# Optimization experiments

Measured on AMD Instinct MI355X. Metric: run time of the kernel, lower is better.

## Reference

```python
import jax, jax.numpy as jnp
import numpy as np

B, N, OBS, H, A = 1024, 64, 128, 256, 16
NH = 4
HD = H // NH


def _linear_params(key, fan_in, fan_out):
    k1, k2 = jax.random.split(key)
    bound = 1.0 / np.sqrt(fan_in)
    W = jax.random.uniform(k1, (fan_out, fan_in), jnp.float32, -bound, bound)
    b = jax.random.uniform(k2, (fan_out,), jnp.float32, -bound, bound)
    return W, b


def setup_inputs() -> dict:
    key = jax.random.key(0)
    ks = jax.random.split(key, 10)
    obs = jax.random.normal(ks[0], (B, N, OBS), jnp.float32)
    adj = jax.random.randint(ks[1], (B, N, N), 0, 2).astype(jnp.float32)
    # guarantee every row has at least one neighbor (self-loop) so softmax is finite
    adj = jnp.maximum(adj, jnp.eye(N, dtype=jnp.float32)[None])
    W1, b1 = _linear_params(ks[2], OBS, H)
    W2, b2 = _linear_params(ks[3], H, H)
    Wq, bq = _linear_params(ks[4], H, H)
    Wk, bk = _linear_params(ks[5], H, H)
    Wv, bv = _linear_params(ks[6], H, H)
    Wo, bo = _linear_params(ks[7], H, H)
    Wc, bc = _linear_params(ks[8], H, H)
    W3, b3 = _linear_params(ks[9], H, A)
    return dict(obs=obs, adj=adj, W1=W1, b1=b1, W2=W2, b2=b2,
                Wq=Wq, bq=bq, Wk=Wk, bk=bk, Wv=Wv, bv=bv,
                Wo=Wo, bo=bo, Wc=Wc, bc=bc, W3=W3, b3=b3)


def reference(obs, adj, W1, b1, W2, b2, Wq, bq, Wk, bk, Wv, bv, Wo, bo, Wc, bc, W3, b3):
    lin = lambda x, W, b: jnp.einsum('bnd,od->bno', x, W) + b
    x = jax.nn.relu(lin(obs, W1, b1))
    x = jax.nn.relu(lin(x, W2, b2))
    # multi-head attention with adjacency mask
    def heads(t):  # [B,N,H] -> [B,NH,N,HD]
        return t.reshape(B, N, NH, HD).transpose(0, 2, 1, 3)
    q = heads(lin(x, Wq, bq))
    k = heads(lin(x, Wk, bk))
    v = heads(lin(x, Wv, bv))
    scores = jnp.einsum('bhqd,bhkd->bhqk', q, k) / np.sqrt(HD).astype(np.float32)
    scores = jnp.where(adj[:, None] == 0, -jnp.inf, scores)
    attn = jax.nn.softmax(scores, axis=-1)
    out = jnp.einsum('bhqk,bhkd->bhqd', attn, v)
    out = out.transpose(0, 2, 1, 3).reshape(B, N, H)
    x = lin(out, Wo, bo)
    # communication: adj @ fc(x)
    x = jnp.einsum('bnm,bmh->bnh', adj, lin(x, Wc, bc))
    return lin(x, W3, b3)
```

## Files before the change

kernel.cpp:

```cpp
#include <hip/hip_runtime.h>
#include <stdint.h>

typedef unsigned short u16;
typedef unsigned long long u64;
typedef __attribute__((ext_vector_type(8))) short short8;
typedef __attribute__((ext_vector_type(4))) float f32x4;

#define MFMA16 __builtin_amdgcn_mfma_f32_16x16x32_bf16

#define MTOT 65536

__device__ __forceinline__ u16 f2bf(float f) {
  union { float f; uint32_t u; } v; v.f = f;
  uint32_t r = v.u + 0x7FFFu + ((v.u >> 16) & 1u);
  return (u16)(r >> 16);
}

union U8 { short8 v; u16 u[8]; };
union U4 { u64 v; u16 u[4]; };

__device__ __forceinline__ void cp16(const void* g, void* l) {
  __builtin_amdgcn_global_load_lds(
      (const __attribute__((address_space(1))) void*)g,
      (__attribute__((address_space(3))) void*)l, 16, 0, 0);
}

__device__ __forceinline__ int swz(int row) { return ((row >> 1) & 3) << 4; }

__global__ __launch_bounds__(256) void k_l1(
    const float* __restrict__ Wc, const float* __restrict__ Wo,
    const float* __restrict__ bo, const float* __restrict__ bc,
    float* __restrict__ M1, float* __restrict__ bv,
    const float* __restrict__ W1, const float* __restrict__ W2,
    const float* __restrict__ Wq, const float* __restrict__ Wk,
    u16* o1, u16* o2, u16* oq, u16* ok,
    const float* __restrict__ adj, u64* __restrict__ adjm_g) {
  const int bid = blockIdx.x, tid = threadIdx.x;
  if (bid < 256) {
    __shared__ float wcr[256];
    __shared__ float red[4];
    const int j = bid, d = tid;
    wcr[d] = Wc[j * 256 + d];
    __syncthreads();
    float acc = 0.f;
#pragma unroll 8
    for (int i = 0; i < 256; i++) acc += wcr[i] * Wo[i * 256 + d];
    M1[j * 256 + d] = acc;
    float p = wcr[d] * bo[d];
    for (int off = 32; off >= 1; off >>= 1) p += __shfl_xor(p, off);
    if ((d & 63) == 0) red[d >> 6] = p;
    __syncthreads();
    if (d == 0) bv[j] = bc[j] + red[0] + red[1] + red[2] + red[3];
  } else if (bid < 368) {
    int off8 = (bid - 256) * 256 + tid;
    const float* src; u16* dst;
    if      (off8 <  4096) { src = W1; dst = o1; }
    else if (off8 < 12288) { src = W2; dst = o2; off8 -= 4096; }
    else if (off8 < 20480) { src = Wq; dst = oq; off8 -= 12288; }
    else                   { src = Wk; dst = ok; off8 -= 20480; }
    const int e = off8 * 8;
    f32x4 a = *(const f32x4*)(src + e);
    f32x4 b = *(const f32x4*)(src + e + 4);
    U8 pk;
#pragma unroll
    for (int j = 0; j < 4; j++) { pk.u[j] = f2bf(a[j]); pk.u[4 + j] = f2bf(b[j]); }
    *(short8*)(dst + e) = pk.v;
  } else {
    __shared__ u16 chunk[64][4];
    const int b = bid - 368;
    const int q = tid >> 2, qa = tid & 3;
    const float* ar = adj + ((size_t)b * 64 + q) * 64 + qa * 16;
    f32x4 a0 = *(const f32x4*)(ar);
    f32x4 a1 = *(const f32x4*)(ar + 4);
    f32x4 a2 = *(const f32x4*)(ar + 8);
    f32x4 a3 = *(const f32x4*)(ar + 12);
    unsigned m16 = 0;
#pragma unroll
    for (int i = 0; i < 4; i++) {
      m16 |= (unsigned)(a0[i] != 0.f) << i;
      m16 |= (unsigned)(a1[i] != 0.f) << (4 + i);
      m16 |= (unsigned)(a2[i] != 0.f) << (8 + i);
      m16 |= (unsigned)(a3[i] != 0.f) << (12 + i);
    }
    chunk[q][qa] = (u16)m16;
    __syncthreads();
    if (tid < 64)
      adjm_g[(size_t)b * 64 + tid] =
          (u64)chunk[tid][0] | ((u64)chunk[tid][1] << 16) |
          ((u64)chunk[tid][2] << 32) | ((u64)chunk[tid][3] << 48);
  }
}

template<int K, bool AF32, bool VZ>
__device__ __forceinline__ void gemm_full2(
    const void* __restrict__ Ain, const u16* __restrict__ W,
    const float* __restrict__ bias, u16* __restrict__ C,
    const int m0, const bool relu, char* smem,
    const u16* __restrict__ Gw, u16* __restrict__ Vzt) {
  const int tid = threadIdx.x;
  const int lane = tid & 63, wid = tid >> 6;
  const int wr = wid >> 1, wc = wid & 1;
  const int ro = lane & 15, hi = lane >> 4;

  f32x4 acc0[4][4], acc1[4][4];
#pragma unroll
  for (int m = 0; m < 4; m++)
#pragma unroll
    for (int n = 0; n < 4; n++) {
      acc0[m][n] = (f32x4){0.f, 0.f, 0.f, 0.f};
      acc1[m][n] = (f32x4){0.f, 0.f, 0.f, 0.f};
    }
  f32x4 vzacc[2][4];
  if (VZ) {
#pragma unroll
    for (int h = 0; h < 2; h++)
#pragma unroll
      for (int cf = 0; cf < 4; cf++) vzacc[h][cf] = (f32x4){0.f, 0.f, 0.f, 0.f};
  }

  auto stage = [&](int buf, int k0) {
    char* Ax = smem + buf * 24576;
    char* Bx = Ax + 8192;
    if (AF32) {
      const float* Af = (const float*)Ain;
#pragma unroll
      for (int it = 0; it < 2; it++) {
        const int e = (tid + it * 256) * 8;
        const int r = e >> 5, c = e & 31;
        const float* s = Af + (size_t)(m0 + r) * K + k0 + c;
        f32x4 a = *(const f32x4*)s, b = *(const f32x4*)(s + 4);
        U8 pk;
#pragma unroll
        for (int j = 0; j < 4; j++) { pk.u[j] = f2bf(a[j]); pk.u[4 + j] = f2bf(b[j]); }
        *(short8*)(Ax + ((r * 64 + c * 2) ^ swz(r))) = pk.v;
      }
    } else {
      const u16* Ab = (const u16*)Ain;
#pragma unroll
      for (int i = 0; i < 2; i++) {
        const int boff = i * 4096 + wid * 1024;
        const int t = boff + lane * 16;
        const int row = t >> 6;
        const int cb = (t & 63) ^ swz(row);
        cp16(Ab + (size_t)(m0 + row) * K + k0 + (cb >> 1), Ax + boff);
      }
    }
#pragma unroll
    for (int i = 0; i < 4; i++) {
      const int boff = i * 4096 + wid * 1024;
      const int t = boff + lane * 16;
      const int row = t >> 6;
      const int cb = (t & 63) ^ swz(row);
      cp16(W + (size_t)row * K + k0 + (cb >> 1), Bx + boff);
    }
  };

  auto compute = [&](int buf) {
    char* Ax = smem + buf * 24576;
    char* Bx = Ax + 8192;
    short8 af[4], fb0[4], fb1[4];
#pragma unroll
    for (int m = 0; m < 4; m++) {
      const int row = wr * 64 + m * 16 + ro;
      af[m] = *(const short8*)(Ax + ((row * 64 + hi * 16) ^ swz(row)));
    }
#pragma unroll
    for (int n = 0; n < 4; n++) {
      const int r0 = wc * 64 + n * 16 + ro;
      fb0[n] = *(const short8*)(Bx + ((r0 * 64 + hi * 16) ^ swz(r0)));
      const int r1 = 128 + r0;
      fb1[n] = *(const short8*)(Bx + ((r1 * 64 + hi * 16) ^ swz(r1)));
    }
    __builtin_amdgcn_s_setprio(1);
#pragma unroll
    for (int m = 0; m < 4; m++)
#pragma unroll
      for (int n = 0; n < 4; n++) {
        acc0[m][n] = MFMA16(af[m], fb0[n], acc0[m][n], 0, 0, 0);
        acc1[m][n] = MFMA16(af[m], fb1[n], acc1[m][n], 0, 0, 0);
      }
    __builtin_amdgcn_s_setprio(0);
  };

  constexpr int NT = K / 32;
  if (AF32) {
    stage(0, 0);
    __syncthreads();
    int cur = 0;
    for (int k0 = 32; k0 < K; k0 += 32) {
      stage(cur ^ 1, k0);
      compute(cur);
      __syncthreads();
      cur ^= 1;
    }
    compute(cur);
    __syncthreads();
  } else {
    stage(0, 0);
    stage(1, 32);
#pragma unroll
    for (int t = 0; t < NT; ++t) {
      if (t == NT - 1) asm volatile("s_waitcnt vmcnt(0)" ::: "memory");
      else             asm volatile("s_waitcnt vmcnt(6)" ::: "memory");
      asm volatile("s_barrier" ::: "memory");
      compute(t & 1);
      asm volatile("s_barrier" ::: "memory");
      if (t + 2 < NT) stage(t & 1, (t + 2) * 32);
    }
  }

  u16 (*Cs)[136] = (u16(*)[136])smem;
  char* Gl = smem + 18432;
  auto ep = [&](f32x4 (&acc)[4][4], const int n0) {
    if (VZ) {
#pragma unroll
      for (int i = 0; i < 4; i++) {
        const int boff = i * 4096 + wid * 1024;
        const int t = boff + lane * 16;
        const int row = t >> 8;
        const int cb = (t & 255) ^ ((row & 7) << 4);
        cp16(Gw + (size_t)row * 256 + n0 + (cb >> 1), Gl + boff);
      }
    }
#pragma unroll
    for (int half = 0; half < 2; half++) {
      if (wr == half) {
#pragma unroll
        for (int n = 0; n < 4; n++) {
          const int col = wc * 64 + n * 16 + ro;
          const float bb = bias[n0 + col];
#pragma unroll
          for (int m = 0; m < 4; m++)
#pragma unroll
            for (int j = 0; j < 4; j++) {
              float val = acc[m][n][j] + bb;
              if (relu) val = fmaxf(val, 0.f);
              Cs[m * 16 + hi * 4 + j][col] = f2bf(val);
            }
        }
      }
      __syncthreads();
      for (int i = tid; i < 64 * 16; i += 256) {
        const int r = i >> 4, c = (i & 15) << 3;
        *(short8*)(C + (size_t)(m0 + half * 64 + r) * 256 + n0 + c) = *(short8*)&Cs[r][c];
      }
      if (VZ) {
#pragma unroll
        for (int ks = 0; ks < 4; ks++) {
          short8 af = *(const short8*)&Cs[wid * 16 + ro][ks * 32 + hi * 8];
#pragma unroll
          for (int cf = 0; cf < 4; cf++) {
            const int c = cf * 16 + ro;
            short8 gb = *(const short8*)(Gl + ((c * 256 + (ks * 32 + hi * 8) * 2) ^ ((c & 7) << 4)));
            vzacc[half][cf] = MFMA16(af, gb, vzacc[half][cf], 0, 0, 0);
          }
        }
      }
      __syncthreads();
    }
  };
  ep(acc0, 0);
  ep(acc1, 128);

  if (VZ) {
#pragma unroll
    for (int half = 0; half < 2; half++) {
      const int bidx = (m0 >> 6) + half;
      const int ke = wid * 16 + hi * 4;
#pragma unroll
      for (int cf = 0; cf < 4; cf++) {
        const int c = cf * 16 + ro;
        U4 pk;
#pragma unroll
        for (int j = 0; j < 4; j++) pk.u[j] = f2bf(vzacc[half][cf][j]);
        *(u64*)(Vzt + (size_t)bidx * 4096 + (size_t)c * 64 + ke) = pk.v;
      }
    }
  }
}

__global__ __launch_bounds__(256, 2) void k_gemm1_prep2(
    const float* __restrict__ obs, const u16* __restrict__ W1b,
    const float* __restrict__ b1, u16* __restrict__ x1,
    const float* __restrict__ W3, const float* __restrict__ M1,
    const float* __restrict__ bvchain, const float* __restrict__ bvw,
    const float* __restrict__ Wv, u16* __restrict__ G,
    float* __restrict__ bz) {
  __shared__ char smem[49152];
  if (blockIdx.x < 512) {
    gemm_full2<128, true, false>(obs, W1b, b1, x1, (int)blockIdx.x * 128,
                                 true, smem, nullptr, nullptr);
    return;
  }
  float* w3r = (float*)smem;
  float* wzs = (float*)(smem + 1024);
  float* red = (float*)(smem + 2048);
  const int a = blockIdx.x - 512, d = threadIdx.x;
  w3r[d] = W3[a * 256 + d];
  __syncthreads();
  float acc = 0.f;
#pragma unroll 8
  for (int j = 0; j < 256; j++) acc += w3r[j] * M1[j * 256 + d];
  wzs[d] = acc;
  float p = w3r[d] * bvchain[d] + acc * bvw[d];
  for (int off = 32; off >= 1; off >>= 1) p += __shfl_xor(p, off);
  if ((d & 63) == 0) red[d >> 6] = p;
  __syncthreads();
  if (d == 0) bz[a] = red[0] + red[1] + red[2] + red[3];
#pragma unroll
  for (int h = 0; h < 4; h++) {
    float g = 0.f;
#pragma unroll 8
    for (int d2 = 0; d2 < 64; d2++)
      g += wzs[h * 64 + d2] * Wv[(size_t)(h * 64 + d2) * 256 + d];
    G[(size_t)(h * 16 + a) * 256 + d] = f2bf(g);
  }
}

__global__ __launch_bounds__(256, 2) void k_x2_vz(
    const u16* __restrict__ x1, const u16* __restrict__ W2b,
    const float* __restrict__ b2, u16* __restrict__ x2,
    const u16* __restrict__ G, u16* __restrict__ Vzt) {
  __shared__ char smem[49152];
  gemm_full2<256, false, true>(x1, W2b, b2, x2, (int)blockIdx.x * 128,
                               true, smem, G, Vzt);
}

__global__ __launch_bounds__(256, 2) void k_qk(
    const u16* __restrict__ x2,
    const u16* __restrict__ Wqb, const float* __restrict__ bq, u16* __restrict__ Qg,
    const u16* __restrict__ Wkb, const float* __restrict__ bk, u16* __restrict__ Kg) {
  __shared__ char smem[49152];
  const int bid = blockIdx.x;
  const int q = bid >> 4, r = bid & 15;
  const int mt = q * 8 + (r & 7);
  const int sub = r >> 3;
  gemm_full2<256, false, false>(x2, sub ? Wkb : Wqb, sub ? bk : bq,
                                sub ? Kg : Qg, mt * 128, false, smem,
                                nullptr, nullptr);
}

__global__ __launch_bounds__(256, 2) void attn_fused(
    const u16* __restrict__ Qg, const u16* __restrict__ Kg,
    const u16* __restrict__ Vzt, const u64* __restrict__ adjm_g,
    const float* __restrict__ bz, const float* __restrict__ b3,
    float* __restrict__ out) {
  __shared__ char sm_raw[36864];
  __shared__ u64 adjm[64];
  u16 (*Ps)[64][72] = (u16(*)[64][72])sm_raw;
  float (*Zs)[64][16] = (float(*)[64][16])sm_raw;

  const int b = blockIdx.x, tid = threadIdx.x;
  const int lane = tid & 63, w = tid >> 6;
  const int ro = lane & 15, hi = lane >> 4;
  const int hc = w * 64;
  const size_t base = (size_t)b * 64 * 256;

  if (tid < 64) adjm[tid] = adjm_g[(size_t)b * 64 + tid];

  short8 kb[4][2];
#pragma unroll
  for (int n = 0; n < 4; n++)
#pragma unroll
    for (int ks = 0; ks < 2; ks++)
      kb[n][ks] = *(const short8*)(Kg + base + (size_t)(n * 16 + ro) * 256 + hc + ks * 32 + hi * 8);

  f32x4 s[4][4];
#pragma unroll
  for (int m = 0; m < 4; m++) {
    short8 af[2];
#pragma unroll
    for (int ks = 0; ks < 2; ks++)
      af[ks] = *(const short8*)(Qg + base + (size_t)(m * 16 + ro) * 256 + hc + ks * 32 + hi * 8);
#pragma unroll
    for (int n = 0; n < 4; n++) s[m][n] = (f32x4){0.f, 0.f, 0.f, 0.f};
#pragma unroll
    for (int ks = 0; ks < 2; ks++)
#pragma unroll
      for (int n = 0; n < 4; n++)
        s[m][n] = MFMA16(af[ks], kb[n][ks], s[m][n], 0, 0, 0);
  }

  short8 vz[2];
#pragma unroll
  for (int ks = 0; ks < 2; ks++)
    vz[ks] = *(const short8*)(Vzt + (size_t)b * 4096 + (size_t)(hc / 4 + ro) * 64 + ks * 32 + hi * 8);

  __syncthreads();

#pragma unroll
  for (int m = 0; m < 4; m++) {
#pragma unroll
    for (int j = 0; j < 4; j++) {
      const int q = m * 16 + hi * 4 + j;
      const u64 msk = adjm[q];
      float sv[4], ev[4];
      float mx = -3.0e38f;
#pragma unroll
      for (int n = 0; n < 4; n++) {
        const bool on = (msk >> (n * 16 + ro)) & 1ull;
        sv[n] = on ? s[m][n][j] * 0.125f : -3.0e38f;
        mx = fmaxf(mx, sv[n]);
      }
      mx = fmaxf(mx, __shfl_xor(mx, 1));
      mx = fmaxf(mx, __shfl_xor(mx, 2));
      mx = fmaxf(mx, __shfl_xor(mx, 4));
      mx = fmaxf(mx, __shfl_xor(mx, 8));
      float sum = 0.f;
#pragma unroll
      for (int n = 0; n < 4; n++) {
        ev[n] = (sv[n] > -1.0e37f) ? __expf(sv[n] - mx) : 0.f;
        sum += ev[n];
      }
      sum += __shfl_xor(sum, 1);
      sum += __shfl_xor(sum, 2);
      sum += __shfl_xor(sum, 4);
      sum += __shfl_xor(sum, 8);
      const float inv = 1.0f / sum;
#pragma unroll
      for (int n = 0; n < 4; n++)
        Ps[w][q][n * 16 + ro] = f2bf(ev[n] * inv);
    }
  }

  f32x4 oz[4];
#pragma unroll
  for (int m = 0; m < 4; m++) {
    short8 pa[2];
    pa[0] = *(const short8*)&Ps[w][m * 16 + ro][hi * 8];
    pa[1] = *(const short8*)&Ps[w][m * 16 + ro][32 + hi * 8];
    oz[m] = (f32x4){0.f, 0.f, 0.f, 0.f};
#pragma unroll
    for (int ks = 0; ks < 2; ks++)
      oz[m] = MFMA16(pa[ks], vz[ks], oz[m], 0, 0, 0);
  }
  __syncthreads();

#pragma unroll
  for (int m = 0; m < 4; m++)
#pragma unroll
    for (int j = 0; j < 4; j++)
      Zs[w][m * 16 + hi * 4 + j][ro] = oz[m][j];
  __syncthreads();

  for (int i = tid; i < 1024; i += 256) {
    const int r = i >> 4, a = i & 15;
    Zs[0][r][a] += Zs[1][r][a] + Zs[2][r][a] + Zs[3][r][a];
  }
  __syncthreads();

  {
    const int n = tid >> 2, a4 = (tid & 3) << 2;
    const u64 msk = adjm[n];
    const float deg = (float)__popcll(msk);
    float a0 = 0.f, a1 = 0.f, a2 = 0.f, a3 = 0.f;
#pragma unroll 8
    for (int m = 0; m < 64; m++) {
      const float wv = (float)((msk >> m) & 1ull);
      f32x4 z = *(const f32x4*)&Zs[0][m][a4];
      a0 += wv * z[0]; a1 += wv * z[1]; a2 += wv * z[2]; a3 += wv * z[3];
    }
    f32x4 r;
    r[0] = a0 + b3[a4 + 0] + deg * bz[a4 + 0];
    r[1] = a1 + b3[a4 + 1] + deg * bz[a4 + 1];
    r[2] = a2 + b3[a4 + 2] + deg * bz[a4 + 2];
    r[3] = a3 + b3[a4 + 3] + deg * bz[a4 + 3];
    *(f32x4*)(out + ((size_t)b * 64 + n) * 16 + a4) = r;
  }
}

extern "C" void kernel_launch(void* const* d_in, const int* in_sizes, int n_in,
                              void* d_out, int out_size, void* d_ws, size_t ws_size,
                              hipStream_t stream) {
  const float* obs = (const float*)d_in[0];
  const float* adj = (const float*)d_in[1];
  const float* W1  = (const float*)d_in[2];
  const float* b1  = (const float*)d_in[3];
  const float* W2  = (const float*)d_in[4];
  const float* b2  = (const float*)d_in[5];
  const float* Wq  = (const float*)d_in[6];
  const float* bq  = (const float*)d_in[7];
  const float* Wk  = (const float*)d_in[8];
  const float* bk  = (const float*)d_in[9];
  const float* Wv  = (const float*)d_in[10];
  const float* bvw = (const float*)d_in[11];
  const float* Wo  = (const float*)d_in[12];
  const float* bo  = (const float*)d_in[13];
  const float* Wc  = (const float*)d_in[14];
  const float* bc  = (const float*)d_in[15];
  const float* W3  = (const float*)d_in[16];
  const float* b3  = (const float*)d_in[17];
  float* out = (float*)d_out;

  char* ws = (char*)d_ws;
  const size_t BIG = (size_t)MTOT * 256 * 2;
  u16* buf0 = (u16*)(ws);
  u16* buf1 = (u16*)(ws + BIG);
  u16* buf2 = (u16*)(ws + 2 * BIG);
  u16* buf3 = (u16*)(ws + 3 * BIG);
  char* p = ws + 4 * BIG;
  u16* W1b = (u16*)p;              p += 128 * 256 * 2;
  u16* W2b = (u16*)p;              p += 256 * 256 * 2;
  u16* Wqb = (u16*)p;              p += 256 * 256 * 2;
  u16* Wkb = (u16*)p;              p += 256 * 256 * 2;
  float* M1 = (float*)p;           p += 256 * 256 * 4;
  u16* G   = (u16*)p;              p += 64 * 256 * 2;
  float* bv = (float*)p;           p += 256 * 4;
  float* bz = (float*)p;           p += 16 * 4;
  u64* adjm_g = (u64*)p;           p += (size_t)MTOT * 8;
  u16* Vzt = (u16*)p;              p += (size_t)MTOT * 64 * 2;

  dim3 blk(256);
  k_l1<<<dim3(1392), blk, 0, stream>>>(Wc, Wo, bo, bc, M1, bv,
                                       W1, W2, Wq, Wk, W1b, W2b, Wqb, Wkb,
                                       adj, adjm_g);
  k_gemm1_prep2<<<dim3(528), blk, 0, stream>>>(obs, W1b, b1, buf0,
                                               W3, M1, bv, bvw, Wv, G, bz);
  k_x2_vz<<<dim3(512), blk, 0, stream>>>(buf0, W2b, b2, buf1, G, Vzt);
  k_qk<<<dim3(1024), blk, 0, stream>>>(buf1, Wqb, bq, buf2, Wkb, bk, buf3);
  attn_fused<<<dim3(1024), blk, 0, stream>>>(buf2, buf3, Vzt, adjm_g, bz, b3, out);
}
```

Baseline: 130.1 us.

## Move Vz projection into Q-GEMM main loop and split G precompute across kernels

The Vz = x2·Gᵀ product was computed in the x2 GEMM epilogue from freshly written bf16 tiles. It now runs inside the K-loop of the Q-projection blocks in k_qk, reusing the already loaded x2 A-fragments with G tiles staged alongside the weights. The G matrix computation is split: Wz is stored to global in the prep kernel and G is built by extra blocks in the x2 kernel. This shortens the x2 epilogue and spreads the small prep work, but Q blocks do extra MFMAs and loads, and shared memory rises to 56KB, which may limit occupancy.

```diff
diff --git a/kernel.cpp b/kernel.cpp
--- a/kernel.cpp
+++ b/kernel.cpp
@@ -110,12 +110,12 @@
       acc0[m][n] = (f32x4){0.f, 0.f, 0.f, 0.f};
       acc1[m][n] = (f32x4){0.f, 0.f, 0.f, 0.f};
     }
-  f32x4 vzacc[2][4];
+  f32x4 vzacc[4][2];
   if (VZ) {
 #pragma unroll
-    for (int h = 0; h < 2; h++)
-#pragma unroll
-      for (int cf = 0; cf < 4; cf++) vzacc[h][cf] = (f32x4){0.f, 0.f, 0.f, 0.f};
+    for (int m = 0; m < 4; m++)
+#pragma unroll
+      for (int cf = 0; cf < 2; cf++) vzacc[m][cf] = (f32x4){0.f, 0.f, 0.f, 0.f};
   }
 
   auto stage = [&](int buf, int k0) {
@@ -153,6 +153,14 @@
       const int cb = (t & 63) ^ swz(row);
       cp16(W + (size_t)row * K + k0 + (cb >> 1), Bx + boff);
     }
+    if (VZ) {
+      char* Gx = smem + 49152 + buf * 4096;
+      const int boff = wid * 1024;
+      const int t = boff + lane * 16;
+      const int row = t >> 6;
+      const int cb = (t & 63) ^ swz(row);
+      cp16(Gw + (size_t)row * 256 + k0 + (cb >> 1), Gx + boff);
+    }
   };
 
   auto compute = [&](int buf) {
@@ -179,6 +187,17 @@
         acc0[m][n] = MFMA16(af[m], fb0[n], acc0[m][n], 0, 0, 0);
         acc1[m][n] = MFMA16(af[m], fb1[n], acc1[m][n], 0, 0, 0);
       }
+    if (VZ) {
+      char* Gx = smem + 49152 + buf * 4096;
+#pragma unroll
+      for (int cf = 0; cf < 2; cf++) {
+        const int row = wc * 32 + cf * 16 + ro;
+        short8 gb = *(const short8*)(Gx + ((row * 64 + hi * 16) ^ swz(row)));
+#pragma unroll
+        for (int m = 0; m < 4; m++)
+          vzacc[m][cf] = MFMA16(af[m], gb, vzacc[m][cf], 0, 0, 0);
+      }
+    }
     __builtin_amdgcn_s_setprio(0);
   };
 
@@ -200,8 +219,9 @@
     stage(1, 32);
 #pragma unroll
     for (int t = 0; t < NT; ++t) {
-      if (t == NT - 1) asm volatile("s_waitcnt vmcnt(0)" ::: "memory");
-      else             asm volatile("s_waitcnt vmcnt(6)" ::: "memory");
+      if (t == NT - 1)  asm volatile("s_waitcnt vmcnt(0)" ::: "memory");
+      else if (VZ)      asm volatile("s_waitcnt vmcnt(7)" ::: "memory");
+      else              asm volatile("s_waitcnt vmcnt(6)" ::: "memory");
       asm volatile("s_barrier" ::: "memory");
       compute(t & 1);
       asm volatile("s_barrier" ::: "memory");
@@ -209,19 +229,24 @@
     }
   }
 
+  if (VZ) {
+#pragma unroll
+    for (int m = 0; m < 4; m++) {
+      const int bidx = (m0 >> 6) + wr;
+      const int ke = m * 16 + hi * 4;
+#pragma unroll
+      for (int cf = 0; cf < 2; cf++) {
+        const int c = wc * 32 + cf * 16 + ro;
+        U4 pk;
+#pragma unroll
+        for (int j = 0; j < 4; j++) pk.u[j] = f2bf(vzacc[m][cf][j]);
+        *(u64*)(Vzt + (size_t)bidx * 4096 + (size_t)c * 64 + ke) = pk.v;
+      }
+    }
+  }
+
   u16 (*Cs)[136] = (u16(*)[136])smem;
-  char* Gl = smem + 18432;
   auto ep = [&](f32x4 (&acc)[4][4], const int n0) {
-    if (VZ) {
-#pragma unroll
-      for (int i = 0; i < 4; i++) {
-        const int boff = i * 4096 + wid * 1024;
-        const int t = boff + lane * 16;
-        const int row = t >> 8;
-        const int cb = (t & 255) ^ ((row & 7) << 4);
-        cp16(Gw + (size_t)row * 256 + n0 + (cb >> 1), Gl + boff);
-      }
-    }
 #pragma unroll
     for (int half = 0; half < 2; half++) {
       if (wr == half) {
@@ -244,39 +269,11 @@
         const int r = i >> 4, c = (i & 15) << 3;
         *(short8*)(C + (size_t)(m0 + half * 64 + r) * 256 + n0 + c) = *(short8*)&Cs[r][c];
       }
-      if (VZ) {
-#pragma unroll
-        for (int ks = 0; ks < 4; ks++) {
-          short8 af = *(const short8*)&Cs[wid * 16 + ro][ks * 32 + hi * 8];
-#pragma unroll
-          for (int cf = 0; cf < 4; cf++) {
-            const int c = cf * 16 + ro;
-            short8 gb = *(const short8*)(Gl + ((c * 256 + (ks * 32 + hi * 8) * 2) ^ ((c & 7) << 4)));
-            vzacc[half][cf] = MFMA16(af, gb, vzacc[half][cf], 0, 0, 0);
-          }
-        }
-      }
       __syncthreads();
     }
   };
   ep(acc0, 0);
   ep(acc1, 128);
-
-  if (VZ) {
-#pragma unroll
-    for (int half = 0; half < 2; half++) {
-      const int bidx = (m0 >> 6) + half;
-      const int ke = wid * 16 + hi * 4;
-#pragma unroll
-      for (int cf = 0; cf < 4; cf++) {
-        const int c = cf * 16 + ro;
-        U4 pk;
-#pragma unroll
-        for (int j = 0; j < 4; j++) pk.u[j] = f2bf(vzacc[half][cf][j]);
-        *(u64*)(Vzt + (size_t)bidx * 4096 + (size_t)c * 64 + ke) = pk.v;
-      }
-    }
-  }
 }
 
 __global__ __launch_bounds__(256, 2) void k_gemm1_prep2(
@@ -284,8 +281,7 @@
     const float* __restrict__ b1, u16* __restrict__ x1,
     const float* __restrict__ W3, const float* __restrict__ M1,
     const float* __restrict__ bvchain, const float* __restrict__ bvw,
-    const float* __restrict__ Wv, u16* __restrict__ G,
-    float* __restrict__ bz) {
+    float* __restrict__ Wzf, float* __restrict__ bz) {
   __shared__ char smem[49152];
   if (blockIdx.x < 512) {
     gemm_full2<128, true, false>(obs, W1b, b1, x1, (int)blockIdx.x * 128,
@@ -293,51 +289,60 @@
     return;
   }
   float* w3r = (float*)smem;
-  float* wzs = (float*)(smem + 1024);
-  float* red = (float*)(smem + 2048);
+  float* red = (float*)(smem + 1024);
   const int a = blockIdx.x - 512, d = threadIdx.x;
   w3r[d] = W3[a * 256 + d];
   __syncthreads();
   float acc = 0.f;
 #pragma unroll 8
   for (int j = 0; j < 256; j++) acc += w3r[j] * M1[j * 256 + d];
-  wzs[d] = acc;
+  Wzf[a * 256 + d] = acc;
   float p = w3r[d] * bvchain[d] + acc * bvw[d];
   for (int off = 32; off >= 1; off >>= 1) p += __shfl_xor(p, off);
   if ((d & 63) == 0) red[d >> 6] = p;
   __syncthreads();
   if (d == 0) bz[a] = red[0] + red[1] + red[2] + red[3];
-#pragma unroll
-  for (int h = 0; h < 4; h++) {
-    float g = 0.f;
-#pragma unroll 8
-    for (int d2 = 0; d2 < 64; d2++)
-      g += wzs[h * 64 + d2] * Wv[(size_t)(h * 64 + d2) * 256 + d];
-    G[(size_t)(h * 16 + a) * 256 + d] = f2bf(g);
-  }
-}
-
-__global__ __launch_bounds__(256, 2) void k_x2_vz(
+}
+
+__global__ __launch_bounds__(256, 2) void k_x2_prep3(
     const u16* __restrict__ x1, const u16* __restrict__ W2b,
     const float* __restrict__ b2, u16* __restrict__ x2,
-    const u16* __restrict__ G, u16* __restrict__ Vzt) {
+    const float* __restrict__ Wzf, const float* __restrict__ Wv,
+    u16* __restrict__ G) {
   __shared__ char smem[49152];
-  gemm_full2<256, false, true>(x1, W2b, b2, x2, (int)blockIdx.x * 128,
-                               true, smem, G, Vzt);
+  if (blockIdx.x < 512) {
+    gemm_full2<256, false, false>(x1, W2b, b2, x2, (int)blockIdx.x * 128,
+                                  true, smem, nullptr, nullptr);
+    return;
+  }
+  const int g = blockIdx.x - 512, d2 = threadIdx.x;
+  const int h = g >> 4, a = g & 15;
+  float* wzr = (float*)smem;
+  if (d2 < 64) wzr[d2] = Wzf[a * 256 + h * 64 + d2];
+  __syncthreads();
+  float acc = 0.f;
+#pragma unroll 8
+  for (int d = 0; d < 64; d++) acc += wzr[d] * Wv[(size_t)(h * 64 + d) * 256 + d2];
+  G[g * 256 + d2] = f2bf(acc);
 }
 
 __global__ __launch_bounds__(256, 2) void k_qk(
     const u16* __restrict__ x2,
     const u16* __restrict__ Wqb, const float* __restrict__ bq, u16* __restrict__ Qg,
-    const u16* __restrict__ Wkb, const float* __restrict__ bk, u16* __restrict__ Kg) {
-  __shared__ char smem[49152];
+    const u16* __restrict__ Wkb, const float* __restrict__ bk, u16* __restrict__ Kg,
+    const u16* __restrict__ G, u16* __restrict__ Vzt) {
+  __shared__ char smem[57344];
   const int bid = blockIdx.x;
   const int q = bid >> 4, r = bid & 15;
   const int mt = q * 8 + (r & 7);
   const int sub = r >> 3;
-  gemm_full2<256, false, false>(x2, sub ? Wkb : Wqb, sub ? bk : bq,
-                                sub ? Kg : Qg, mt * 128, false, smem,
-                                nullptr, nullptr);
+  if (sub == 0) {
+    gemm_full2<256, false, true>(x2, Wqb, bq, Qg, mt * 128, false, smem,
+                                 G, Vzt);
+  } else {
+    gemm_full2<256, false, false>(x2, Wkb, bk, Kg, mt * 128, false, smem,
+                                  nullptr, nullptr);
+  }
 }
 
 __global__ __launch_bounds__(256, 2) void attn_fused(
@@ -504,6 +509,7 @@
   u16* Wqb = (u16*)p;              p += 256 * 256 * 2;
   u16* Wkb = (u16*)p;              p += 256 * 256 * 2;
   float* M1 = (float*)p;           p += 256 * 256 * 4;
+  float* Wzf = (float*)p;          p += 16 * 256 * 4;
   u16* G   = (u16*)p;              p += 64 * 256 * 2;
   float* bv = (float*)p;           p += 256 * 4;
   float* bz = (float*)p;           p += 16 * 4;
@@ -515,8 +521,9 @@
                                        W1, W2, Wq, Wk, W1b, W2b, Wqb, Wkb,
                                        adj, adjm_g);
   k_gemm1_prep2<<<dim3(528), blk, 0, stream>>>(obs, W1b, b1, buf0,
-                                               W3, M1, bv, bvw, Wv, G, bz);
-  k_x2_vz<<<dim3(512), blk, 0, stream>>>(buf0, W2b, b2, buf1, G, Vzt);
-  k_qk<<<dim3(1024), blk, 0, stream>>>(buf1, Wqb, bq, buf2, Wkb, bk, buf3);
+                                               W3, M1, bv, bvw, Wzf, bz);
+  k_x2_prep3<<<dim3(576), blk, 0, stream>>>(buf0, W2b, b2, buf1, Wzf, Wv, G);
+  k_qk<<<dim3(1024), blk, 0, stream>>>(buf1, Wqb, bq, buf2, Wkb, bk, buf3,
+                                       G, Vzt);
   attn_fused<<<dim3(1024), blk, 0, stream>>>(buf2, buf3, Vzt, adjm_g, bz, b3, out);
 }
```

New measurement: 125.0 us. -3.9%, faster.
